# Optimization experiments

Measured on AMD Instinct MI355X. Metric: run time of the kernel, lower is better.

Reference implementation:

```python
import jax, jax.numpy as jnp
import numpy as np

LN_EPS = 1e-12  # config.layer_norm_eps (BERT default)


def setup_inputs() -> dict:
    key = jax.random.key(0)
    k1, k2, k3, k4 = jax.random.split(key, 4)
    B, S, D_IN, D_OUT = 16, 512, 4096, 1024
    return {
        "hidden_states": jax.random.normal(k1, (B, S, D_IN), dtype=jnp.float32),
        "input_tensor": jax.random.normal(k2, (B, S, D_OUT), dtype=jnp.float32),
        "W": jax.random.normal(k3, (D_OUT, D_IN), dtype=jnp.float32) * 0.02,
        "b": jax.random.normal(k4, (D_OUT,), dtype=jnp.float32) * 0.02,
        "gamma": jnp.ones((D_OUT,), dtype=jnp.float32),
        "beta": jnp.zeros((D_OUT,), dtype=jnp.float32),
    }


def reference(hidden_states, input_tensor, W, b, gamma, beta):
    # mix_Linear 1-bit path (XNOR-Net style): binarize weights with per-row scale
    alpha = jnp.mean(jnp.abs(W), axis=1, keepdims=True)   # [D_OUT, 1]
    W_q = jnp.sign(W) * alpha                              # [D_OUT, D_IN]
    # dense GEMM: [B,S,D_IN] x [D_OUT,D_IN]^T -> [B,S,D_OUT]
    h = jnp.einsum("bsi,oi->bso", hidden_states, W_q) + b
    # dropout is identity in eval mode; residual add + LayerNorm
    x = h + input_tensor
    mu = jnp.mean(x, axis=-1, keepdims=True)
    var = jnp.mean(jnp.square(x - mu), axis=-1, keepdims=True)
    return gamma * (x - mu) * jax.lax.rsqrt(var + LN_EPS) + beta
```

## Files before the change

### kernel.cpp

```cpp
#include <hip/hip_runtime.h>

using u16    = unsigned short;
using short8 = __attribute__((ext_vector_type(8))) short;
using u16x8  = __attribute__((ext_vector_type(8))) u16;
using u16x4  = __attribute__((ext_vector_type(4))) u16;
using f32x4  = __attribute__((ext_vector_type(4))) float;

#define M_DIM 8192
#define N_DIM 1024
#define K_DIM 4096

typedef __attribute__((address_space(1))) void gvoid;
typedef __attribute__((address_space(3))) void svoid;
#define GLOAD_LDS16(g, s) \
  __builtin_amdgcn_global_load_lds((gvoid*)(void*)(g), (svoid*)(s), 16, 0, 0)

__device__ __forceinline__ u16 f2bf(float f) {
  unsigned u = __builtin_bit_cast(unsigned, f);
  u = (u + 0x7FFFu + ((u >> 16) & 1u)) >> 16;
  return (u16)u;
}

__global__ __launch_bounds__(256) void wprep_kernel(const float* __restrict__ W,
                                                    u16* __restrict__ Wsgn,
                                                    float* __restrict__ alpha) {
  const int row = blockIdx.x;
  const int t   = threadIdx.x;
  const float4* wr = (const float4*)(W + (size_t)row * K_DIM);
  float4 v[4];
  float s = 0.f;
#pragma unroll
  for (int j = 0; j < 4; ++j) {
    v[j] = wr[t + 256 * j];
    s += fabsf(v[j].x) + fabsf(v[j].y) + fabsf(v[j].z) + fabsf(v[j].w);
  }
#pragma unroll
  for (int off = 32; off > 0; off >>= 1) s += __shfl_down(s, off, 64);
  __shared__ float red[4];
  if ((t & 63) == 0) red[t >> 6] = s;
  __syncthreads();
  if (t == 0) alpha[row] = (red[0] + red[1] + red[2] + red[3]) * (1.0f / K_DIM);
  u16x4* dst = (u16x4*)(Wsgn + (size_t)row * K_DIM);
#pragma unroll
  for (int j = 0; j < 4; ++j) {
    u16x4 sg;
    sg[0] = v[j].x > 0.f ? 0x3F80 : (v[j].x < 0.f ? 0xBF80 : 0);
    sg[1] = v[j].y > 0.f ? 0x3F80 : (v[j].y < 0.f ? 0xBF80 : 0);
    sg[2] = v[j].z > 0.f ? 0x3F80 : (v[j].z < 0.f ? 0xBF80 : 0);
    sg[3] = v[j].w > 0.f ? 0x3F80 : (v[j].w < 0.f ? 0xBF80 : 0);
    dst[t + 256 * j] = sg;
  }
}

__global__ __launch_bounds__(256) void cast_kernel(const float* __restrict__ in,
                                                   u16* __restrict__ out) {
  const size_t i = ((size_t)blockIdx.x * 256 + threadIdx.x) * 8;
  float4 a = ((const float4*)(in + i))[0];
  float4 b = ((const float4*)(in + i))[1];
  u16x8 p;
  p[0] = f2bf(a.x); p[1] = f2bf(a.y); p[2] = f2bf(a.z); p[3] = f2bf(a.w);
  p[4] = f2bf(b.x); p[5] = f2bf(b.y); p[6] = f2bf(b.z); p[7] = f2bf(b.w);
  *(u16x8*)(out + i) = p;
}

template <bool PRE>
__global__ __launch_bounds__(256) void gemm_kernel(const void* __restrict__ Aopaque,
                                                   const u16* __restrict__ Bsgn,
                                                   const float* __restrict__ alpha,
                                                   const float* __restrict__ bias,
                                                   const float* __restrict__ resid,
                                                   float* __restrict__ out) {
  __shared__ u16 lA[2][128 * 64];
  __shared__ u16 lB[2][128 * 64];
  const int tid  = threadIdx.x;
  const int wave = tid >> 6;
  const int lane = tid & 63;
  const int quad = lane >> 4;
  const int l16  = lane & 15;
  const int wm   = (wave >> 1) * 64;
  const int wn   = (wave & 1) * 64;

  const int b    = blockIdx.x;
  const int xcd  = b & 7;
  const int l    = b >> 3;
  const size_t m0 = (size_t)(xcd * 8 + (l >> 3)) * 128;
  const size_t n0 = (size_t)(l & 7) * 128;

  f32x4 acc[4][4] = {};

  const int r8  = lane >> 3;
  const int kgs = ((lane & 7) ^ r8) * 8;
  const u16* bsrc[4];
  const u16* asrc16[4];
  int        coff[4];
#pragma unroll
  for (int j = 0; j < 4; ++j) {
    const int c = wave * 4 + j;
    bsrc[j] = Bsgn + (n0 + (size_t)c * 8 + r8) * K_DIM + kgs;
    if constexpr (PRE)
      asrc16[j] = (const u16*)Aopaque + (m0 + (size_t)c * 8 + r8) * K_DIM + kgs;
    coff[j] = c * 512;
  }

#define STAGE(K0, BUF)                                                         \
  do {                                                                         \
    _Pragma("unroll")                                                          \
    for (int j = 0; j < 4; ++j) GLOAD_LDS16(bsrc[j] + (K0), &lB[BUF][coff[j]]); \
    if constexpr (PRE) {                                                       \
      _Pragma("unroll")                                                        \
      for (int j = 0; j < 4; ++j) GLOAD_LDS16(asrc16[j] + (K0), &lA[BUF][coff[j]]); \
    } else {                                                                   \
      const float* Af = (const float*)Aopaque;                                 \
      const int row = tid >> 1;                                                \
      const int h   = tid & 1;                                                 \
      _Pragma("unroll")                                                        \
      for (int g = 0; g < 4; ++g) {                                            \
        const int kg = h * 4 + g;                                              \
        const float4* src = (const float4*)(Af + (m0 + row) * (size_t)K_DIM +  \
                                            (K0) + kg * 8);                    \
        float4 f0 = src[0], f1 = src[1];                                       \
        u16x8 p;                                                               \
        p[0] = f2bf(f0.x); p[1] = f2bf(f0.y); p[2] = f2bf(f0.z); p[3] = f2bf(f0.w); \
        p[4] = f2bf(f1.x); p[5] = f2bf(f1.y); p[6] = f2bf(f1.z); p[7] = f2bf(f1.w); \
        *(u16x8*)(&lA[BUF][row * 64 + ((kg ^ (row & 7)) * 8)]) = p;            \
      }                                                                        \
    }                                                                          \
  } while (0)

#define COMPUTE(BUF)                                                           \
  do {                                                                         \
    _Pragma("unroll")                                                          \
    for (int s = 0; s < 2; ++s) {                                              \
      const int kq = s * 4 + quad;                                             \
      short8 af[4], bf[4];                                                     \
      _Pragma("unroll")                                                        \
      for (int mt = 0; mt < 4; ++mt) {                                         \
        const int row = wm + mt * 16 + l16;                                    \
        af[mt] = *(const short8*)(&lA[BUF][row * 64 + ((kq ^ (row & 7)) * 8)]); \
      }                                                                        \
      _Pragma("unroll")                                                        \
      for (int nt = 0; nt < 4; ++nt) {                                         \
        const int col = wn + nt * 16 + l16;                                    \
        bf[nt] = *(const short8*)(&lB[BUF][col * 64 + ((kq ^ (col & 7)) * 8)]); \
      }                                                                        \
      _Pragma("unroll")                                                        \
      for (int mt = 0; mt < 4; ++mt)                                           \
        _Pragma("unroll")                                                      \
        for (int nt = 0; nt < 4; ++nt)                                         \
          acc[mt][nt] = __builtin_amdgcn_mfma_f32_16x16x32_bf16(af[mt], bf[nt], \
                                                                acc[mt][nt], 0, 0, 0); \
    }                                                                          \
  } while (0)

  STAGE(0, 0);
  __syncthreads();

  int cur = 0;
#pragma unroll 1
  for (int k0 = 0; k0 < K_DIM - 64; k0 += 64) {
    STAGE(k0 + 64, cur ^ 1);
    COMPUTE(cur);
    __syncthreads();
    cur ^= 1;
  }
  COMPUTE(cur);

#pragma unroll
  for (int nt = 0; nt < 4; ++nt) {
    const size_t n  = n0 + wn + nt * 16 + l16;
    const float  al = alpha[n];
    const float  bi = bias[n];
#pragma unroll
    for (int mt = 0; mt < 4; ++mt) {
      const size_t mbase = m0 + wm + mt * 16 + quad * 4;
#pragma unroll
      for (int r = 0; r < 4; ++r) {
        const size_t mm = mbase + r;
        out[mm * N_DIM + n] = acc[mt][nt][r] * al + bi + resid[mm * N_DIM + n];
      }
    }
  }
#undef STAGE
#undef COMPUTE
}

__global__ __launch_bounds__(256) void ln_kernel(float* __restrict__ x,
                                                 const float* __restrict__ gamma,
                                                 const float* __restrict__ beta) {
  const size_t row = blockIdx.x;
  float4* xr = (float4*)(x + row * N_DIM);
  const int t = threadIdx.x;
  float4 v = xr[t];
  float s  = v.x + v.y + v.z + v.w;
  float sq = v.x * v.x + v.y * v.y + v.z * v.z + v.w * v.w;
#pragma unroll
  for (int off = 32; off > 0; off >>= 1) {
    s  += __shfl_down(s, off, 64);
    sq += __shfl_down(sq, off, 64);
  }
  __shared__ float rs[4], rq[4];
  if ((t & 63) == 0) { rs[t >> 6] = s; rq[t >> 6] = sq; }
  __syncthreads();
  s  = rs[0] + rs[1] + rs[2] + rs[3];
  sq = rq[0] + rq[1] + rq[2] + rq[3];
  const float mu  = s * (1.0f / N_DIM);
  float var = sq * (1.0f / N_DIM) - mu * mu;
  var = fmaxf(var, 0.0f);
  const float inv = rsqrtf(var + 1e-12f);
  const float4 g = ((const float4*)gamma)[t];
  const float4 b = ((const float4*)beta)[t];
  v.x = g.x * ((v.x - mu) * inv) + b.x;
  v.y = g.y * ((v.y - mu) * inv) + b.y;
  v.z = g.z * ((v.z - mu) * inv) + b.z;
  v.w = g.w * ((v.w - mu) * inv) + b.w;
  xr[t] = v;
}

extern "C" void kernel_launch(void* const* d_in, const int* in_sizes, int n_in,
                              void* d_out, int out_size, void* d_ws, size_t ws_size,
                              hipStream_t stream) {
  const float* hidden = (const float*)d_in[0];
  const float* resid  = (const float*)d_in[1];
  const float* W      = (const float*)d_in[2];
  const float* bias   = (const float*)d_in[3];
  const float* gamma  = (const float*)d_in[4];
  const float* beta   = (const float*)d_in[5];
  float* out = (float*)d_out;

  char* ws = (char*)d_ws;
  u16*   Wsgn  = (u16*)ws;
  float* alpha = (float*)(ws + 8ull * 1024 * 1024);
  u16*   Abf   = (u16*)(ws + 8ull * 1024 * 1024 + 4096);
  const size_t need_full = 8ull * 1024 * 1024 + 4096 + 64ull * 1024 * 1024;

  wprep_kernel<<<N_DIM, 256, 0, stream>>>(W, Wsgn, alpha);

  const int nblocks = (N_DIM / 128) * (M_DIM / 128);
  if (ws_size >= need_full) {
    cast_kernel<<<(M_DIM * (size_t)K_DIM) / (256 * 8), 256, 0, stream>>>(hidden, Abf);
    gemm_kernel<true><<<nblocks, 256, 0, stream>>>((const void*)Abf, Wsgn, alpha,
                                                   bias, resid, out);
  } else {
    gemm_kernel<false><<<nblocks, 256, 0, stream>>>((const void*)hidden, Wsgn, alpha,
                                                    bias, resid, out);
  }
  ln_kernel<<<M_DIM, 256, 0, stream>>>(out, gamma, beta);
}
```

Baseline: 350.3 us.

## Use 4-stage LDS ring with K=32 slices and explicit vmcnt waits

After: 350.9 us. About the same (+0.2%).

```diff
diff --git a/kernel.cpp b/kernel.cpp
--- a/kernel.cpp
+++ b/kernel.cpp
@@ -70,8 +70,8 @@
                                                    const float* __restrict__ bias,
                                                    const float* __restrict__ resid,
                                                    float* __restrict__ out) {
-  __shared__ u16 lA[2][128 * 64];
-  __shared__ u16 lB[2][128 * 64];
+  __shared__ u16 lA[4][128 * 32];
+  __shared__ u16 lB[4][128 * 32];
   const int tid  = threadIdx.x;
   const int wave = tid >> 6;
   const int lane = tid & 63;
@@ -88,82 +88,106 @@
 
   f32x4 acc[4][4] = {};
 
-  const int r8  = lane >> 3;
-  const int kgs = ((lane & 7) ^ r8) * 8;
-  const u16* bsrc[4];
-  const u16* asrc16[4];
-  int        coff[4];
-#pragma unroll
-  for (int j = 0; j < 4; ++j) {
-    const int c = wave * 4 + j;
-    bsrc[j] = Bsgn + (n0 + (size_t)c * 8 + r8) * K_DIM + kgs;
+  const int r16 = lane >> 2;
+  const int sl  = lane & 3;
+  const int g   = sl ^ ((r16 ^ (r16 >> 2)) & 3);
+  const u16* bsrc[2];
+  const u16* asrc16[2];
+  int        coff[2];
+#pragma unroll
+  for (int j = 0; j < 2; ++j) {
+    const int c   = wave * 2 + j;
+    const int row = c * 16 + r16;
+    bsrc[j] = Bsgn + (n0 + (size_t)row) * K_DIM + g * 8;
     if constexpr (PRE)
-      asrc16[j] = (const u16*)Aopaque + (m0 + (size_t)c * 8 + r8) * K_DIM + kgs;
-    coff[j] = c * 512;
-  }
+      asrc16[j] = (const u16*)Aopaque + (m0 + (size_t)row) * K_DIM + g * 8;
+    coff[j] = c * 512 + lane * 8;
+  }
+
+  const int fx    = (l16 ^ (l16 >> 2)) & 3;
+  const int slot8 = (quad ^ fx) * 8;
 
 #define STAGE(K0, BUF)                                                         \
   do {                                                                         \
-    _Pragma("unroll")                                                          \
-    for (int j = 0; j < 4; ++j) GLOAD_LDS16(bsrc[j] + (K0), &lB[BUF][coff[j]]); \
+    u16* __a = &lA[BUF][0];                                                    \
+    u16* __b = &lB[BUF][0];                                                    \
+    GLOAD_LDS16(bsrc[0] + (K0), __b + coff[0]);                                \
+    GLOAD_LDS16(bsrc[1] + (K0), __b + coff[1]);                                \
     if constexpr (PRE) {                                                       \
-      _Pragma("unroll")                                                        \
-      for (int j = 0; j < 4; ++j) GLOAD_LDS16(asrc16[j] + (K0), &lA[BUF][coff[j]]); \
+      GLOAD_LDS16(asrc16[0] + (K0), __a + coff[0]);                            \
+      GLOAD_LDS16(asrc16[1] + (K0), __a + coff[1]);                            \
     } else {                                                                   \
       const float* Af = (const float*)Aopaque;                                 \
       const int row = tid >> 1;                                                \
       const int h   = tid & 1;                                                 \
+      const int xv  = (row ^ (row >> 2)) & 3;                                  \
       _Pragma("unroll")                                                        \
-      for (int g = 0; g < 4; ++g) {                                            \
-        const int kg = h * 4 + g;                                              \
+      for (int gg = 0; gg < 2; ++gg) {                                         \
+        const int kg = h * 2 + gg;                                             \
         const float4* src = (const float4*)(Af + (m0 + row) * (size_t)K_DIM +  \
                                             (K0) + kg * 8);                    \
         float4 f0 = src[0], f1 = src[1];                                       \
         u16x8 p;                                                               \
         p[0] = f2bf(f0.x); p[1] = f2bf(f0.y); p[2] = f2bf(f0.z); p[3] = f2bf(f0.w); \
         p[4] = f2bf(f1.x); p[5] = f2bf(f1.y); p[6] = f2bf(f1.z); p[7] = f2bf(f1.w); \
-        *(u16x8*)(&lA[BUF][row * 64 + ((kg ^ (row & 7)) * 8)]) = p;            \
+        *(u16x8*)(__a + row * 32 + ((kg ^ xv) * 8)) = p;                       \
       }                                                                        \
     }                                                                          \
   } while (0)
 
+#define WAIT_STEADY()                                                          \
+  do {                                                                         \
+    if constexpr (PRE) asm volatile("s_waitcnt vmcnt(8)" ::: "memory");        \
+    else asm volatile("s_waitcnt vmcnt(0) lgkmcnt(0)" ::: "memory");           \
+  } while (0)
+
+#define WAIT_N(N)                                                              \
+  do {                                                                         \
+    if constexpr (PRE) asm volatile("s_waitcnt vmcnt(" #N ")" ::: "memory");   \
+    else asm volatile("s_waitcnt vmcnt(0) lgkmcnt(0)" ::: "memory");           \
+  } while (0)
+
+#define BARRIER()                                                              \
+  do {                                                                         \
+    __builtin_amdgcn_s_barrier();                                              \
+    asm volatile("" ::: "memory");                                             \
+  } while (0)
+
 #define COMPUTE(BUF)                                                           \
   do {                                                                         \
+    const u16* __a = &lA[BUF][0];                                              \
+    const u16* __b = &lB[BUF][0];                                              \
+    short8 af[4], bf[4];                                                       \
     _Pragma("unroll")                                                          \
-    for (int s = 0; s < 2; ++s) {                                              \
-      const int kq = s * 4 + quad;                                             \
-      short8 af[4], bf[4];                                                     \
+    for (int mt = 0; mt < 4; ++mt)                                             \
+      af[mt] = *(const short8*)(__a + (wm + mt * 16 + l16) * 32 + slot8);      \
+    _Pragma("unroll")                                                          \
+    for (int nt = 0; nt < 4; ++nt)                                             \
+      bf[nt] = *(const short8*)(__b + (wn + nt * 16 + l16) * 32 + slot8);      \
+    _Pragma("unroll")                                                          \
+    for (int mt = 0; mt < 4; ++mt)                                             \
       _Pragma("unroll")                                                        \
-      for (int mt = 0; mt < 4; ++mt) {                                         \
-        const int row = wm + mt * 16 + l16;                                    \
-        af[mt] = *(const short8*)(&lA[BUF][row * 64 + ((kq ^ (row & 7)) * 8)]); \
-      }                                                                        \
-      _Pragma("unroll")                                                        \
-      for (int nt = 0; nt < 4; ++nt) {                                         \
-        const int col = wn + nt * 16 + l16;                                    \
-        bf[nt] = *(const short8*)(&lB[BUF][col * 64 + ((kq ^ (col & 7)) * 8)]); \
-      }                                                                        \
-      _Pragma("unroll")                                                        \
-      for (int mt = 0; mt < 4; ++mt)                                           \
-        _Pragma("unroll")                                                      \
-        for (int nt = 0; nt < 4; ++nt)                                         \
-          acc[mt][nt] = __builtin_amdgcn_mfma_f32_16x16x32_bf16(af[mt], bf[nt], \
-                                                                acc[mt][nt], 0, 0, 0); \
-    }                                                                          \
+      for (int nt = 0; nt < 4; ++nt)                                           \
+        acc[mt][nt] = __builtin_amdgcn_mfma_f32_16x16x32_bf16(af[mt], bf[nt],  \
+                                                              acc[mt][nt], 0, 0, 0); \
   } while (0)
 
   STAGE(0, 0);
-  __syncthreads();
-
-  int cur = 0;
+  STAGE(32, 1);
+
 #pragma unroll 1
-  for (int k0 = 0; k0 < K_DIM - 64; k0 += 64) {
-    STAGE(k0 + 64, cur ^ 1);
-    COMPUTE(cur);
-    __syncthreads();
-    cur ^= 1;
-  }
-  COMPUTE(cur);
+  for (int j = 0; j < 126; ++j) {
+    STAGE((j + 2) * 32, (j + 2) & 3);
+    WAIT_STEADY();
+    BARRIER();
+    COMPUTE(j & 3);
+  }
+  WAIT_N(4);
+  BARRIER();
+  COMPUTE(2);
+  WAIT_N(0);
+  BARRIER();
+  COMPUTE(3);
 
 #pragma unroll
   for (int nt = 0; nt < 4; ++nt) {
@@ -181,6 +205,9 @@
     }
   }
 #undef STAGE
+#undef WAIT_STEADY
+#undef WAIT_N
+#undef BARRIER
 #undef COMPUTE
 }
 
```
